# Performance work log

Hardware: AMD Instinct MI355X
Metric: run time of the kernel (lower is better)

## Reference

```python
import jax, jax.numpy as jnp
import numpy as np

D_MODEL = 1024
NUM_HEADS = 16
SCALE = 1.0 / np.sqrt(D_MODEL // NUM_HEADS)  # matches sqrt(d_model // num_heads)


def setup_inputs() -> dict:
    key = jax.random.key(0)
    ks = jax.random.split(key, 7)
    B, S, D = 4, 2048, D_MODEL
    std = 1.0 / np.sqrt(D)
    return {
        "x": jax.random.normal(ks[0], (B, S, D), dtype=jnp.float32),
        "Wq": jax.random.normal(ks[1], (D, D), dtype=jnp.float32) * std,
        "bq": jnp.zeros((D,), dtype=jnp.float32),
        "Wk": jax.random.normal(ks[2], (D, D), dtype=jnp.float32) * std,
        "bk": jnp.zeros((D,), dtype=jnp.float32),
        "Wv": jax.random.normal(ks[3], (D, D), dtype=jnp.float32) * std,
        "bv": jnp.zeros((D,), dtype=jnp.float32),
    }


def reference(x, Wq, bq, Wk, bk, Wv, bv):
    # QKV projections (nn.Linear: x @ W^T + b; here W stored as [in, out] already)
    Q = x @ Wq + bq  # [B, S, D]
    K = x @ Wk + bk
    V = x @ Wv + bv
    scores = jnp.einsum("bsd,btd->bst", Q, K) * SCALE  # [B, S, S]
    S_len = x.shape[1]
    causal = jnp.tril(jnp.ones((S_len, S_len), dtype=bool))
    scores = jnp.where(causal, scores, -jnp.inf)
    attn = jax.nn.softmax(scores, axis=-1)
    return jnp.einsum("bst,btd->bsd", attn, V)
```

## Files before the change

kernel.cpp:

```cpp
#include <hip/hip_runtime.h>
#include <hip/hip_bf16.h>
#include <cstdint>

#define D_MODEL 1024
#define SEQ     2048
#define SCALE   0.125f
#define P_ELEMS 2228224

typedef __attribute__((ext_vector_type(8))) _Float16 f16x8;
typedef __attribute__((ext_vector_type(8))) unsigned short u16x8;
typedef __attribute__((ext_vector_type(4))) unsigned short u16x4;
typedef __attribute__((ext_vector_type(4))) float f32x4;

__device__ __forceinline__ unsigned short f2h(float f) {
  _Float16 h = (_Float16)f;
  return __builtin_bit_cast(unsigned short, h);
}

__device__ __forceinline__ void gll16(const void* g, void* lds_p) {
  __builtin_amdgcn_global_load_lds(
      (const __attribute__((address_space(1))) unsigned int*)(uintptr_t)g,
      (__attribute__((address_space(3))) unsigned int*)(unsigned int)(uintptr_t)lds_p,
      16, 0, 0);
}

#define WAITV8 asm volatile("s_waitcnt vmcnt(8)" ::: "memory")
#define WAITV0 asm volatile("s_waitcnt vmcnt(0)" ::: "memory")
#define WAITL0 asm volatile("s_waitcnt lgkmcnt(0)" ::: "memory")
#define SCHEDB __builtin_amdgcn_sched_barrier(0)
#define BAR    __builtin_amdgcn_s_barrier()

__device__ __forceinline__ void stage_tile(const unsigned short* gA, const unsigned short* gB,
                                           size_t sA, size_t sB,
                                           int k0, unsigned short* buf, int w, int lane) {
  int rl = lane >> 3;
  int sg = ((lane & 7) ^ rl) << 3;
#pragma unroll
  for (int j = 0; j < 4; j++) {
    int c = w * 4 + j;
    int row = c * 8 + rl;
    gll16(gA + (size_t)row * sA + k0 + sg, buf + c * 512);
    gll16(gB + (size_t)row * sB + k0 + sg, buf + 8192 + c * 512);
  }
}

__device__ __forceinline__ void load_frags(const unsigned short* buf, int wr, int wc,
                                           int l15, int l4, f16x8 af[4][2], f16x8 bf[4][2]) {
  const unsigned short* bA = buf;
  const unsigned short* bB = buf + 8192;
#pragma unroll
  for (int m = 0; m < 4; m++) {
    int row = wr * 64 + m * 16 + l15, rs = row & 7;
    af[m][0] = *(const f16x8*)(bA + row * 64 + ((l4 ^ rs) << 3));
    af[m][1] = *(const f16x8*)(bA + row * 64 + (((4 + l4) ^ rs) << 3));
  }
#pragma unroll
  for (int n = 0; n < 4; n++) {
    int row = wc * 64 + n * 16 + l15, rs = row & 7;
    bf[n][0] = *(const f16x8*)(bB + row * 64 + ((l4 ^ rs) << 3));
    bf[n][1] = *(const f16x8*)(bB + row * 64 + (((4 + l4) ^ rs) << 3));
  }
}

__device__ __forceinline__ void mfma_tile(f16x8 af[4][2], f16x8 bf[4][2], f32x4 acc[4][4]) {
#pragma unroll
  for (int m = 0; m < 4; m++)
#pragma unroll
    for (int n = 0; n < 4; n++) {
      acc[m][n] = __builtin_amdgcn_mfma_f32_16x16x32_f16(af[m][0], bf[n][0], acc[m][n], 0, 0, 0);
      acc[m][n] = __builtin_amdgcn_mfma_f32_16x16x32_f16(af[m][1], bf[n][1], acc[m][n], 0, 0, 0);
    }
}

__device__ __forceinline__ void gemm_core(const unsigned short* gA, const unsigned short* gB,
                                          size_t sA, size_t sB,
                                          unsigned short* lds0, unsigned short* lds1, int nt,
                                          int w, int lane, int wr, int wc, int l15, int l4,
                                          f32x4 acc[4][4]) {
  stage_tile(gA, gB, sA, sB, 0, lds0, w, lane);
  stage_tile(gA, gB, sA, sB, 64, lds1, w, lane);
  WAITV8; SCHEDB; BAR;
  f16x8 af[4][2], bf[4][2];
  for (int t = 0; t < nt; t += 2) {
    load_frags(lds0, wr, wc, l15, l4, af, bf);
    WAITL0; SCHEDB; BAR;
    if (t + 2 < nt) stage_tile(gA, gB, sA, sB, (t + 2) * 64, lds0, w, lane);
    __builtin_amdgcn_s_setprio(1);
    mfma_tile(af, bf, acc);
    __builtin_amdgcn_s_setprio(0);
    if (t + 2 < nt) { WAITV8; } else { WAITV0; }
    SCHEDB; BAR;
    load_frags(lds1, wr, wc, l15, l4, af, bf);
    WAITL0; SCHEDB; BAR;
    if (t + 3 < nt) stage_tile(gA, gB, sA, sB, (t + 3) * 64, lds1, w, lane);
    __builtin_amdgcn_s_setprio(1);
    mfma_tile(af, bf, acc);
    __builtin_amdgcn_s_setprio(0);
    if (t + 3 < nt) { WAITV8; } else { WAITV0; }
    SCHEDB; BAR;
  }
}

__global__ __launch_bounds__(256) void cvt_x(const float* __restrict__ x,
                                             unsigned short* __restrict__ o, int n8) {
  int i = blockIdx.x * 256 + threadIdx.x;
  if (i >= n8) return;
  const float4* p = (const float4*)x + (size_t)i * 2;
  float4 a = p[0], b = p[1];
  u16x8 r;
  r[0] = f2h(a.x); r[1] = f2h(a.y); r[2] = f2h(a.z); r[3] = f2h(a.w);
  r[4] = f2h(b.x); r[5] = f2h(b.y); r[6] = f2h(b.z); r[7] = f2h(b.w);
  *((u16x8*)o + i) = r;
}

__global__ __launch_bounds__(256) void cvt_w(const float* __restrict__ W0,
                                             const float* __restrict__ W1,
                                             const float* __restrict__ W2,
                                             unsigned short* __restrict__ out) {
  __shared__ float t[32][33];
  int z = blockIdx.z;
  const float* W = (z == 0) ? W0 : (z == 1 ? W1 : W2);
  unsigned short* o = out + (size_t)z * 1024 * 1024;
  int c0 = blockIdx.x * 32, r0 = blockIdx.y * 32;
  int tx = threadIdx.x, ty = threadIdx.y;
  for (int i = 0; i < 4; i++)
    t[ty + 8 * i][tx] = W[(size_t)(r0 + ty + 8 * i) * 1024 + c0 + tx];
  __syncthreads();
  for (int i = 0; i < 4; i++)
    o[(size_t)(c0 + ty + 8 * i) * 1024 + r0 + tx] = f2h(t[tx][ty + 8 * i]);
}

__global__ __launch_bounds__(256) void qkv_gemm(const unsigned short* __restrict__ xb,
                                                const unsigned short* __restrict__ wt,
                                                const float* __restrict__ b0,
                                                const float* __restrict__ b1,
                                                const float* __restrict__ b2,
                                                unsigned short* __restrict__ Qp,
                                                unsigned short* __restrict__ Kp,
                                                unsigned short* __restrict__ vtp) {
  __shared__ unsigned short lds[2][16384];
  int m0 = blockIdx.x * 128;
  int n0 = blockIdx.y * 128;
  int z = n0 >> 10, nz = n0 & 1023;
  const unsigned short* gA = xb + (size_t)m0 * 1024;
  const unsigned short* gB = wt + (size_t)z * 1048576 + (size_t)nz * 1024;
  const float* bias = (z == 0) ? b0 : (z == 1 ? b1 : b2);
  int tid = threadIdx.x, lane = tid & 63, w = tid >> 6;
  int wr = w >> 1, wc = w & 1, l15 = lane & 15, l4 = lane >> 4;
  f32x4 acc[4][4] = {};
  gemm_core(gA, gB, 1024, 1024, &lds[0][0], &lds[1][0], 16, w, lane, wr, wc, l15, l4, acc);

  if (z < 2) {
    unsigned short* O = (z == 0) ? Qp : Kp;
#pragma unroll
    for (int m = 0; m < 4; m++)
#pragma unroll
      for (int n = 0; n < 4; n++) {
        int cl = wc * 64 + n * 16 + l15;
        float bv = bias[nz + cl];
#pragma unroll
        for (int r = 0; r < 4; r++) {
          int row = m0 + wr * 64 + m * 16 + l4 * 4 + r;
          O[(size_t)row * 1024 + nz + cl] = f2h(acc[m][n][r] + bv);
        }
      }
  } else {
    unsigned short* T = &lds[0][0];
#pragma unroll
    for (int m = 0; m < 4; m++)
#pragma unroll
      for (int n = 0; n < 4; n++) {
        int cl = wc * 64 + n * 16 + l15;
        float bv = bias[nz + cl];
#pragma unroll
        for (int r = 0; r < 4; r++) {
          int rl = wr * 64 + m * 16 + l4 * 4 + r;
          T[cl * 136 + rl] = f2h(acc[m][n][r] + bv);
        }
      }
    __syncthreads();
    int bidx = m0 >> 11, s0 = m0 & 2047;
#pragma unroll
    for (int i = 0; i < 8; i++) {
      int d = w * 32 + i * 4 + (lane >> 4);
      int ch = lane & 15;
      u16x8 v = *(const u16x8*)(T + d * 136 + ch * 8);
      *(u16x8*)(vtp + ((size_t)bidx * 1024 + nz + d) * 2048 + s0 + ch * 8) = v;
    }
  }
}

__global__ __launch_bounds__(256) void qk_scores(const unsigned short* __restrict__ Q,
                                                 const unsigned short* __restrict__ Kb,
                                                 float* __restrict__ sc) {
  __shared__ unsigned short lds[2][16384];
  int b = blockIdx.y;
  int i = blockIdx.x;
  int qt = (int)((sqrtf(8.f * i + 1.f) - 1.f) * 0.5f);
  while ((qt + 1) * (qt + 2) / 2 <= i) qt++;
  while (qt * (qt + 1) / 2 > i) qt--;
  int kt = i - qt * (qt + 1) / 2;
  int Wspan = (qt + 1) << 7;
  const unsigned short* gA = Q  + ((size_t)b * 2048 + qt * 128) * 1024;
  const unsigned short* gB = Kb + ((size_t)b * 2048 + kt * 128) * 1024;
  float* outp = sc + (size_t)b * P_ELEMS + (size_t)16384 * (qt * (qt + 1) / 2);
  int tid = threadIdx.x, lane = tid & 63, w = tid >> 6;
  int wr = w >> 1, wc = w & 1, l15 = lane & 15, l4 = lane >> 4;
  f32x4 acc[4][4] = {};
  gemm_core(gA, gB, 1024, 1024, &lds[0][0], &lds[1][0], 16, w, lane, wr, wc, l15, l4, acc);
#pragma unroll
  for (int m = 0; m < 4; m++)
#pragma unroll
    for (int n = 0; n < 4; n++) {
      int cl = wc * 64 + n * 16 + l15;
      int kv = kt * 128 + cl;
#pragma unroll
      for (int r = 0; r < 4; r++) {
        int rl = wr * 64 + m * 16 + l4 * 4 + r;
        int srow = qt * 128 + rl;
        float v = acc[m][n][r] * SCALE;
        if (kv > srow) v = -1e30f;
        outp[(size_t)rl * Wspan + kv] = v;
      }
    }
}

__global__ __launch_bounds__(256) void softmax_row(const float* __restrict__ sc,
                                                   unsigned short* __restrict__ pb) {
  __shared__ float redm[4];
  __shared__ float reds[4];
  int srow = blockIdx.x;
  int b = srow >> 11, sl = srow & 2047;
  int qt = sl >> 7;
  int Wspan = (qt + 1) << 7;
  size_t rb = (size_t)b * P_ELEMS + (size_t)16384 * (qt * (qt + 1) / 2) + (size_t)(sl & 127) * Wspan;
  const float4* src = (const float4*)(sc + rb);
  int nv = Wspan >> 2;
  int t = threadIdx.x, lane = t & 63, w = t >> 6;
  bool h0 = t < nv, h1 = (t + 256) < nv;
  float4 v0 = make_float4(0, 0, 0, 0), v1 = make_float4(0, 0, 0, 0);
  if (h0) v0 = src[t];
  if (h1) v1 = src[t + 256];
  float mx = -1e30f;
  if (h0) mx = fmaxf(fmaxf(v0.x, v0.y), fmaxf(v0.z, v0.w));
  if (h1) mx = fmaxf(mx, fmaxf(fmaxf(v1.x, v1.y), fmaxf(v1.z, v1.w)));
  for (int off = 1; off < 64; off <<= 1) mx = fmaxf(mx, __shfl_xor(mx, off, 64));
  if (lane == 0) redm[w] = mx;
  __syncthreads();
  mx = fmaxf(fmaxf(redm[0], redm[1]), fmaxf(redm[2], redm[3]));
  float s = 0.f;
  float4 e0, e1;
  if (h0) {
    e0.x = __expf(v0.x - mx); e0.y = __expf(v0.y - mx);
    e0.z = __expf(v0.z - mx); e0.w = __expf(v0.w - mx);
    s += e0.x + e0.y + e0.z + e0.w;
  }
  if (h1) {
    e1.x = __expf(v1.x - mx); e1.y = __expf(v1.y - mx);
    e1.z = __expf(v1.z - mx); e1.w = __expf(v1.w - mx);
    s += e1.x + e1.y + e1.z + e1.w;
  }
  for (int off = 1; off < 64; off <<= 1) s += __shfl_xor(s, off, 64);
  if (lane == 0) reds[w] = s;
  __syncthreads();
  s = reds[0] + reds[1] + reds[2] + reds[3];
  float inv = 1.f / s;
  u16x4* dst = (u16x4*)(pb + rb);
  if (h0) {
    u16x4 o;
    o[0] = f2h(e0.x * inv); o[1] = f2h(e0.y * inv);
    o[2] = f2h(e0.z * inv); o[3] = f2h(e0.w * inv);
    dst[t] = o;
  }
  if (h1) {
    u16x4 o;
    o[0] = f2h(e1.x * inv); o[1] = f2h(e1.y * inv);
    o[2] = f2h(e1.z * inv); o[3] = f2h(e1.w * inv);
    dst[t + 256] = o;
  }
}

__global__ __launch_bounds__(256) void pv_gemm(const unsigned short* __restrict__ pb,
                                               const unsigned short* __restrict__ vtp,
                                               float* __restrict__ outp) {
  __shared__ unsigned short lds[2][16384];
  int p = blockIdx.x;
  int n0 = blockIdx.y * 128;
  int b = blockIdx.z;
  int tid = threadIdx.x, lane = tid & 63, w = tid >> 6;
  int wr = w >> 1, wc = w & 1, l15 = lane & 15, l4 = lane >> 4;
  const unsigned short* gB = vtp + (size_t)b * 1024 * 2048 + (size_t)n0 * 2048;
#pragma unroll
  for (int which = 0; which < 2; which++) {
    int qt = which ? (15 - p) : p;
    int Wspan = (qt + 1) << 7;
    const unsigned short* gA = pb + (size_t)b * P_ELEMS + (size_t)16384 * (qt * (qt + 1) / 2);
    float* O = outp + ((size_t)b * 2048 + qt * 128) * 1024;
    f32x4 acc[4][4] = {};
    gemm_core(gA, gB, Wspan, 2048, &lds[0][0], &lds[1][0], 2 * (qt + 1),
              w, lane, wr, wc, l15, l4, acc);
#pragma unroll
    for (int m = 0; m < 4; m++)
#pragma unroll
      for (int n = 0; n < 4; n++) {
        int cl = n0 + wc * 64 + n * 16 + l15;
#pragma unroll
        for (int r = 0; r < 4; r++) {
          int rl = wr * 64 + m * 16 + l4 * 4 + r;
          O[(size_t)rl * 1024 + cl] = acc[m][n][r];
        }
      }
  }
}

extern "C" void kernel_launch(void* const* d_in, const int* in_sizes, int n_in,
                              void* d_out, int out_size, void* d_ws, size_t ws_size,
                              hipStream_t stream) {
  const float* x  = (const float*)d_in[0];
  const float* Wq = (const float*)d_in[1];
  const float* bq = (const float*)d_in[2];
  const float* Wk = (const float*)d_in[3];
  const float* bk = (const float*)d_in[4];
  const float* Wv = (const float*)d_in[5];
  const float* bv = (const float*)d_in[6];
  float* out = (float*)d_out;

  unsigned short* ws  = (unsigned short*)d_ws;
  unsigned short* wt  = ws;
  unsigned short* Qp  = ws + 3145728;
  unsigned short* Kp  = ws + 11534336;
  unsigned short* vtp = ws + 19922944;
  float* sc           = (float*)(ws + 28311552);
  unsigned short* pb  = ws + 46137344;
  unsigned short* xb  = (unsigned short*)d_out;

  cvt_x<<<4096, 256, 0, stream>>>(x, xb, 1048576);
  cvt_w<<<dim3(32, 32, 3), dim3(32, 8), 0, stream>>>(Wq, Wk, Wv, wt);
  qkv_gemm<<<dim3(64, 24), 256, 0, stream>>>(xb, wt, bq, bk, bv, Qp, Kp, vtp);
  qk_scores<<<dim3(136, 4), 256, 0, stream>>>(Qp, Kp, sc);
  softmax_row<<<8192, 256, 0, stream>>>(sc, pb);
  pv_gemm<<<dim3(8, 8, 4), 256, 0, stream>>>(pb, vtp, out);
}
```

Baseline: 156.7 us.

## Store scores in fp16, fuse conversion kernels, swizzle GEMM block order

Result: no change. 157.7 us (+0.7%).

```diff
diff --git a/kernel.cpp b/kernel.cpp
--- a/kernel.cpp
+++ b/kernel.cpp
@@ -9,12 +9,14 @@
 
 typedef __attribute__((ext_vector_type(8))) _Float16 f16x8;
 typedef __attribute__((ext_vector_type(8))) unsigned short u16x8;
-typedef __attribute__((ext_vector_type(4))) unsigned short u16x4;
 typedef __attribute__((ext_vector_type(4))) float f32x4;
 
 __device__ __forceinline__ unsigned short f2h(float f) {
   _Float16 h = (_Float16)f;
   return __builtin_bit_cast(unsigned short, h);
+}
+__device__ __forceinline__ float h2f(unsigned short u) {
+  return (float)__builtin_bit_cast(_Float16, u);
 }
 
 __device__ __forceinline__ void gll16(const void* g, void* lds_p) {
@@ -29,6 +31,7 @@
 #define WAITL0 asm volatile("s_waitcnt lgkmcnt(0)" ::: "memory")
 #define SCHEDB __builtin_amdgcn_sched_barrier(0)
 #define BAR    __builtin_amdgcn_s_barrier()
+#define MFMA16(a, b, c) __builtin_amdgcn_mfma_f32_16x16x32_f16(a, b, c, 0, 0, 0)
 
 __device__ __forceinline__ void stage_tile(const unsigned short* gA, const unsigned short* gB,
                                            size_t sA, size_t sB,
@@ -67,8 +70,8 @@
   for (int m = 0; m < 4; m++)
 #pragma unroll
     for (int n = 0; n < 4; n++) {
-      acc[m][n] = __builtin_amdgcn_mfma_f32_16x16x32_f16(af[m][0], bf[n][0], acc[m][n], 0, 0, 0);
-      acc[m][n] = __builtin_amdgcn_mfma_f32_16x16x32_f16(af[m][1], bf[n][1], acc[m][n], 0, 0, 0);
+      acc[m][n] = MFMA16(af[m][0], bf[n][0], acc[m][n]);
+      acc[m][n] = MFMA16(af[m][1], bf[n][1], acc[m][n]);
     }
 }
 
@@ -101,33 +104,37 @@
   }
 }
 
-__global__ __launch_bounds__(256) void cvt_x(const float* __restrict__ x,
-                                             unsigned short* __restrict__ o, int n8) {
-  int i = blockIdx.x * 256 + threadIdx.x;
-  if (i >= n8) return;
-  const float4* p = (const float4*)x + (size_t)i * 2;
-  float4 a = p[0], b = p[1];
-  u16x8 r;
-  r[0] = f2h(a.x); r[1] = f2h(a.y); r[2] = f2h(a.z); r[3] = f2h(a.w);
-  r[4] = f2h(b.x); r[5] = f2h(b.y); r[6] = f2h(b.z); r[7] = f2h(b.w);
-  *((u16x8*)o + i) = r;
-}
-
-__global__ __launch_bounds__(256) void cvt_w(const float* __restrict__ W0,
-                                             const float* __restrict__ W1,
-                                             const float* __restrict__ W2,
-                                             unsigned short* __restrict__ out) {
+__global__ __launch_bounds__(256) void cvt_fused(const float* __restrict__ x,
+                                                 const float* __restrict__ W0,
+                                                 const float* __restrict__ W1,
+                                                 const float* __restrict__ W2,
+                                                 unsigned short* __restrict__ xb,
+                                                 unsigned short* __restrict__ wt) {
   __shared__ float t[32][33];
-  int z = blockIdx.z;
-  const float* W = (z == 0) ? W0 : (z == 1 ? W1 : W2);
-  unsigned short* o = out + (size_t)z * 1024 * 1024;
-  int c0 = blockIdx.x * 32, r0 = blockIdx.y * 32;
-  int tx = threadIdx.x, ty = threadIdx.y;
-  for (int i = 0; i < 4; i++)
-    t[ty + 8 * i][tx] = W[(size_t)(r0 + ty + 8 * i) * 1024 + c0 + tx];
-  __syncthreads();
-  for (int i = 0; i < 4; i++)
-    o[(size_t)(c0 + ty + 8 * i) * 1024 + r0 + tx] = f2h(t[tx][ty + 8 * i]);
+  int bid = blockIdx.x;
+  int tid = threadIdx.x;
+  if (bid < 4096) {
+    int i = bid * 256 + tid;
+    const float4* p = (const float4*)x + (size_t)i * 2;
+    float4 a = p[0], b = p[1];
+    u16x8 r;
+    r[0] = f2h(a.x); r[1] = f2h(a.y); r[2] = f2h(a.z); r[3] = f2h(a.w);
+    r[4] = f2h(b.x); r[5] = f2h(b.y); r[6] = f2h(b.z); r[7] = f2h(b.w);
+    *((u16x8*)xb + i) = r;
+  } else {
+    int id = bid - 4096;
+    int z = id >> 10, rem = id & 1023;
+    int bx = rem & 31, by = rem >> 5;
+    const float* W = (z == 0) ? W0 : (z == 1 ? W1 : W2);
+    unsigned short* o = wt + (size_t)z * 1048576;
+    int c0 = bx * 32, r0 = by * 32;
+    int tx = tid & 31, ty = tid >> 5;
+    for (int i = 0; i < 4; i++)
+      t[ty + 8 * i][tx] = W[(size_t)(r0 + ty + 8 * i) * 1024 + c0 + tx];
+    __syncthreads();
+    for (int i = 0; i < 4; i++)
+      o[(size_t)(c0 + ty + 8 * i) * 1024 + r0 + tx] = f2h(t[tx][ty + 8 * i]);
+  }
 }
 
 __global__ __launch_bounds__(256) void qkv_gemm(const unsigned short* __restrict__ xb,
@@ -139,8 +146,10 @@
                                                 unsigned short* __restrict__ Kp,
                                                 unsigned short* __restrict__ vtp) {
   __shared__ unsigned short lds[2][16384];
-  int m0 = blockIdx.x * 128;
-  int n0 = blockIdx.y * 128;
+  int lin = blockIdx.y * 64 + blockIdx.x;
+  int swz = (lin & 7) * 192 + (lin >> 3);
+  int m0 = (swz & 63) * 128;
+  int n0 = (swz >> 6) * 128;
   int z = n0 >> 10, nz = n0 & 1023;
   const unsigned short* gA = xb + (size_t)m0 * 1024;
   const unsigned short* gB = wt + (size_t)z * 1048576 + (size_t)nz * 1024;
@@ -192,10 +201,12 @@
 
 __global__ __launch_bounds__(256) void qk_scores(const unsigned short* __restrict__ Q,
                                                  const unsigned short* __restrict__ Kb,
-                                                 float* __restrict__ sc) {
+                                                 unsigned short* __restrict__ sc) {
   __shared__ unsigned short lds[2][16384];
-  int b = blockIdx.y;
-  int i = blockIdx.x;
+  int lin = blockIdx.y * 136 + blockIdx.x;
+  int swz = (lin & 7) * 68 + (lin >> 3);
+  int i = swz % 136;
+  int b = swz / 136;
   int qt = (int)((sqrtf(8.f * i + 1.f) - 1.f) * 0.5f);
   while ((qt + 1) * (qt + 2) / 2 <= i) qt++;
   while (qt * (qt + 1) / 2 > i) qt--;
@@ -203,7 +214,7 @@
   int Wspan = (qt + 1) << 7;
   const unsigned short* gA = Q  + ((size_t)b * 2048 + qt * 128) * 1024;
   const unsigned short* gB = Kb + ((size_t)b * 2048 + kt * 128) * 1024;
-  float* outp = sc + (size_t)b * P_ELEMS + (size_t)16384 * (qt * (qt + 1) / 2);
+  unsigned short* outp = sc + (size_t)b * P_ELEMS + (size_t)16384 * (qt * (qt + 1) / 2);
   int tid = threadIdx.x, lane = tid & 63, w = tid >> 6;
   int wr = w >> 1, wc = w & 1, l15 = lane & 15, l4 = lane >> 4;
   f32x4 acc[4][4] = {};
@@ -219,13 +230,13 @@
         int rl = wr * 64 + m * 16 + l4 * 4 + r;
         int srow = qt * 128 + rl;
         float v = acc[m][n][r] * SCALE;
-        if (kv > srow) v = -1e30f;
-        outp[(size_t)rl * Wspan + kv] = v;
+        if (kv > srow) v = -30000.f;
+        outp[(size_t)rl * Wspan + kv] = f2h(v);
       }
     }
 }
 
-__global__ __launch_bounds__(256) void softmax_row(const float* __restrict__ sc,
+__global__ __launch_bounds__(256) void softmax_row(const unsigned short* __restrict__ sc,
                                                    unsigned short* __restrict__ pb) {
   __shared__ float redm[4];
   __shared__ float reds[4];
@@ -234,49 +245,36 @@
   int qt = sl >> 7;
   int Wspan = (qt + 1) << 7;
   size_t rb = (size_t)b * P_ELEMS + (size_t)16384 * (qt * (qt + 1) / 2) + (size_t)(sl & 127) * Wspan;
-  const float4* src = (const float4*)(sc + rb);
-  int nv = Wspan >> 2;
+  const u16x8* src = (const u16x8*)(sc + rb);
+  int nv = Wspan >> 3;
   int t = threadIdx.x, lane = t & 63, w = t >> 6;
-  bool h0 = t < nv, h1 = (t + 256) < nv;
-  float4 v0 = make_float4(0, 0, 0, 0), v1 = make_float4(0, 0, 0, 0);
-  if (h0) v0 = src[t];
-  if (h1) v1 = src[t + 256];
+  bool h0 = t < nv;
+  float v[8];
   float mx = -1e30f;
-  if (h0) mx = fmaxf(fmaxf(v0.x, v0.y), fmaxf(v0.z, v0.w));
-  if (h1) mx = fmaxf(mx, fmaxf(fmaxf(v1.x, v1.y), fmaxf(v1.z, v1.w)));
+  if (h0) {
+    u16x8 raw = src[t];
+#pragma unroll
+    for (int j = 0; j < 8; j++) { v[j] = h2f(raw[j]); mx = fmaxf(mx, v[j]); }
+  }
   for (int off = 1; off < 64; off <<= 1) mx = fmaxf(mx, __shfl_xor(mx, off, 64));
   if (lane == 0) redm[w] = mx;
   __syncthreads();
   mx = fmaxf(fmaxf(redm[0], redm[1]), fmaxf(redm[2], redm[3]));
   float s = 0.f;
-  float4 e0, e1;
   if (h0) {
-    e0.x = __expf(v0.x - mx); e0.y = __expf(v0.y - mx);
-    e0.z = __expf(v0.z - mx); e0.w = __expf(v0.w - mx);
-    s += e0.x + e0.y + e0.z + e0.w;
-  }
-  if (h1) {
-    e1.x = __expf(v1.x - mx); e1.y = __expf(v1.y - mx);
-    e1.z = __expf(v1.z - mx); e1.w = __expf(v1.w - mx);
-    s += e1.x + e1.y + e1.z + e1.w;
+#pragma unroll
+    for (int j = 0; j < 8; j++) { v[j] = __expf(v[j] - mx); s += v[j]; }
   }
   for (int off = 1; off < 64; off <<= 1) s += __shfl_xor(s, off, 64);
   if (lane == 0) reds[w] = s;
   __syncthreads();
   s = reds[0] + reds[1] + reds[2] + reds[3];
   float inv = 1.f / s;
-  u16x4* dst = (u16x4*)(pb + rb);
   if (h0) {
-    u16x4 o;
-    o[0] = f2h(e0.x * inv); o[1] = f2h(e0.y * inv);
-    o[2] = f2h(e0.z * inv); o[3] = f2h(e0.w * inv);
-    dst[t] = o;
-  }
-  if (h1) {
-    u16x4 o;
-    o[0] = f2h(e1.x * inv); o[1] = f2h(e1.y * inv);
-    o[2] = f2h(e1.z * inv); o[3] = f2h(e1.w * inv);
-    dst[t + 256] = o;
+    u16x8 o;
+#pragma unroll
+    for (int j = 0; j < 8; j++) o[j] = f2h(v[j] * inv);
+    *((u16x8*)(pb + rb) + t) = o;
   }
 }
 
@@ -330,12 +328,11 @@
   unsigned short* Qp  = ws + 3145728;
   unsigned short* Kp  = ws + 11534336;
   unsigned short* vtp = ws + 19922944;
-  float* sc           = (float*)(ws + 28311552);
-  unsigned short* pb  = ws + 46137344;
+  unsigned short* sc  = ws + 28311552;
+  unsigned short* pb  = ws + 37224448;
   unsigned short* xb  = (unsigned short*)d_out;
 
-  cvt_x<<<4096, 256, 0, stream>>>(x, xb, 1048576);
-  cvt_w<<<dim3(32, 32, 3), dim3(32, 8), 0, stream>>>(Wq, Wk, Wv, wt);
+  cvt_fused<<<7168, 256, 0, stream>>>(x, Wq, Wk, Wv, xb, wt);
   qkv_gemm<<<dim3(64, 24), 256, 0, stream>>>(xb, wt, bq, bk, bv, Qp, Kp, vtp);
   qk_scores<<<dim3(136, 4), 256, 0, stream>>>(Qp, Kp, sc);
   softmax_row<<<8192, 256, 0, stream>>>(sc, pb);
```
